# Kernel tuning notes

Measured on AMD Instinct MI355X. Metric: run time of the kernel, lower is better.

The kernel has to match this reference:

```python
import jax, jax.numpy as jnp
import numpy as np

DIM = 2048
H = 16
HD = 128
S = 2640          # frame_seq_len(22*40=880) * num_frame_per_block(3)
CACHE = 5280      # 6 cached frames
MAXPOS = 8192
EPS = 1e-6


def rmsnorm(x, g, eps=EPS):
    return x * jax.lax.rsqrt(jnp.mean(x * x, axis=-1, keepdims=True) + eps) * g


def apply_rope_interleaved(x, cos, sin):
    # x: [s, H, HD]; cos/sin: [s, HD//2]; is_neox=False -> adjacent pairs
    x1 = x[..., 0::2]
    x2 = x[..., 1::2]
    c = cos[:, None, :]
    s_ = sin[:, None, :]
    o1 = x1 * c - x2 * s_
    o2 = x2 * c + x1 * s_
    return jnp.stack([o1, o2], axis=-1).reshape(x.shape)


def setup_inputs() -> dict:
    key = jax.random.key(0)
    ks = jax.random.split(key, 10)
    w_scale = DIM ** -0.5
    x = jax.random.normal(ks[0], (1, S, DIM), dtype=jnp.float32)
    # cos_sin_cache: [max_pos, HD] = [cos(HD//2) | sin(HD//2)], real rope values
    inv_freq = 1.0 / (10000.0 ** (np.arange(0, HD, 2, dtype=np.float32) / HD))
    t = np.arange(MAXPOS, dtype=np.float32)
    ang = np.outer(t, inv_freq)  # [MAXPOS, HD//2]
    freqs = jnp.asarray(np.concatenate([np.cos(ang), np.sin(ang)], axis=1), dtype=jnp.float32)
    k_cache = jax.random.normal(ks[1], (CACHE, H, HD), dtype=jnp.float32)
    v_cache = jax.random.normal(ks[2], (CACHE, H, HD), dtype=jnp.float32)
    Wq = jax.random.normal(ks[3], (DIM, DIM), dtype=jnp.float32) * w_scale
    Wk = jax.random.normal(ks[4], (DIM, DIM), dtype=jnp.float32) * w_scale
    Wv = jax.random.normal(ks[5], (DIM, DIM), dtype=jnp.float32) * w_scale
    Wo = jax.random.normal(ks[6], (DIM, DIM), dtype=jnp.float32) * w_scale
    bq = jnp.zeros((DIM,), jnp.float32)
    bk = jnp.zeros((DIM,), jnp.float32)
    bv = jnp.zeros((DIM,), jnp.float32)
    bo = jnp.zeros((DIM,), jnp.float32)
    gq = jnp.ones((DIM,), jnp.float32)
    gk = jnp.ones((DIM,), jnp.float32)
    return {"x": x, "freqs": freqs, "k_cache": k_cache, "v_cache": v_cache,
            "Wq": Wq, "bq": bq, "Wk": Wk, "bk": bk, "Wv": Wv, "bv": bv,
            "Wo": Wo, "bo": bo, "gq": gq, "gk": gk, "current_start": CACHE}


def reference(x, freqs, k_cache, v_cache, Wq, bq, Wk, bk, Wv, bv, Wo, bo, gq, gk, current_start):
    s = x.shape[1]
    xf = x[0]                                   # [s, DIM], B==1
    q = rmsnorm(xf @ Wq.T + bq, gq).reshape(s, H, HD)
    k = rmsnorm(xf @ Wk.T + bk, gk).reshape(s, H, HD)
    v = (xf @ Wv.T + bv).reshape(s, H, HD)
    # fused RoPE via cos_sin_cache lookup, interleaved (is_neox=False)
    positions = jnp.arange(s, dtype=jnp.int32) + current_start
    cs = freqs[positions]                       # [s, HD]
    cos, sin = cs[:, : HD // 2], cs[:, HD // 2:]
    rq = apply_rope_interleaved(q, cos, sin)
    rk = apply_rope_interleaved(k, cos, sin)
    # streaming attention: full access to cache, causal within incoming block
    k_all = jnp.concatenate([k_cache, rk], axis=0)  # [L, H, HD]
    v_all = jnp.concatenate([v_cache, v], axis=0)
    L = k_all.shape[0]
    scale = HD ** -0.5
    scores = jnp.einsum("qhd,khd->hqk", rq, k_all) * scale  # [H, s, L]
    kv_idx = jnp.arange(L)
    q_idx = jnp.arange(s)
    mask = (kv_idx[None, :] - (L - s)) <= q_idx[:, None]    # cache always visible
    scores = jnp.where(mask[None, :, :], scores, jnp.float32(-1e30))
    attn = jax.nn.softmax(scores, axis=-1)
    out = jnp.einsum("hqk,khd->qhd", attn, v_all).reshape(s, DIM)
    y = out @ Wo.T + bo
    return y[None]                              # [1, s, DIM]
```

## Files before the change

### kernel.cpp

```cpp
#include <hip/hip_runtime.h>

#define DIMN 2048
#define NH 16
#define HDIM 128

typedef __attribute__((ext_vector_type(4))) float f32x4;
typedef __attribute__((ext_vector_type(8))) __bf16 bfx8;
typedef __attribute__((ext_vector_type(8))) unsigned short u16x8;
typedef __attribute__((ext_vector_type(2))) unsigned int u32x2;

__device__ __forceinline__ unsigned short f2bf(float f){
  unsigned u = __builtin_bit_cast(unsigned, f);
  u += 0x7fffu + ((u >> 16) & 1u);
  return (unsigned short)(u >> 16);
}
__device__ __forceinline__ float bf2f(unsigned short h){
  unsigned u = (unsigned)h << 16;
  return __builtin_bit_cast(float, u);
}
__device__ __forceinline__ unsigned cvt_pk_bf16(float lo, float hi){
  unsigned r;
  asm("v_cvt_pk_bf16_f32 %0, %1, %2" : "=v"(r) : "v"(lo), "v"(hi));
  return r;
}

__device__ __forceinline__ void gl_lds16(const void* g, void* l){
  __builtin_amdgcn_global_load_lds((const __attribute__((address_space(1))) void*)g,
                                   (__attribute__((address_space(3))) void*)l, 16, 0, 0);
}

#define MFMA16(a,b,c) __builtin_amdgcn_mfma_f32_16x16x32_bf16((a),(b),(c),0,0,0)

__global__ __launch_bounds__(256) void cast_bf16_kernel(const float* __restrict__ in,
                                                        unsigned short* __restrict__ out, int n8){
  int i = blockIdx.x*256 + threadIdx.x;
  if (i >= n8) return;
  const float4* p = (const float4*)(in + (size_t)i*8);
  float4 a = p[0], b = p[1];
  u16x8 o;
  o[0]=f2bf(a.x); o[1]=f2bf(a.y); o[2]=f2bf(a.z); o[3]=f2bf(a.w);
  o[4]=f2bf(b.x); o[5]=f2bf(b.y); o[6]=f2bf(b.z); o[7]=f2bf(b.w);
  *(u16x8*)(out + (size_t)i*8) = o;
}

__global__ __launch_bounds__(256) void kcache_kernel(const float* __restrict__ kc,
                                                     unsigned short* __restrict__ kb,
                                                     int R, int L_){
  const int gid = blockIdx.x*256 + threadIdx.x;
  if (gid >= R*256) return;
  const size_t idx = (size_t)gid * 8;
  const int k   = (int)(idx >> 11);
  const int rem = (int)(idx & 2047);
  const int hh  = rem >> 7, d = rem & 127;
  const float4* p = (const float4*)(kc + idx);
  float4 a = p[0], b = p[1];
  u16x8 o;
  o[0]=f2bf(a.x); o[1]=f2bf(a.y); o[2]=f2bf(a.z); o[3]=f2bf(a.w);
  o[4]=f2bf(b.x); o[5]=f2bf(b.y); o[6]=f2bf(b.z); o[7]=f2bf(b.w);
  *(u16x8*)(kb + (size_t)hh*L_*HDIM + (size_t)k*HDIM + d) = o;
}

__global__ __launch_bounds__(256) void vtrans_kernel(const float* __restrict__ src,
                                                     unsigned short* __restrict__ vt,
                                                     int R, int koff, int L_){
  __shared__ __align__(16) unsigned short tile[32][72];
  const int kb0 = blockIdx.x * 64, db0 = blockIdx.y * 32, hh = blockIdx.z;
  const int t = threadIdx.x;
  const int kk = t >> 2, dd = (t & 3) * 8;
  const int k = kb0 + kk;
  if (k < R){
    const float* p = src + (size_t)k*DIMN + hh*HDIM + db0 + dd;
    float4 a = ((const float4*)p)[0], b = ((const float4*)p)[1];
    tile[dd+0][kk] = f2bf(a.x); tile[dd+1][kk] = f2bf(a.y);
    tile[dd+2][kk] = f2bf(a.z); tile[dd+3][kk] = f2bf(a.w);
    tile[dd+4][kk] = f2bf(b.x); tile[dd+5][kk] = f2bf(b.y);
    tile[dd+6][kk] = f2bf(b.z); tile[dd+7][kk] = f2bf(b.w);
  }
  __syncthreads();
  const int d = t >> 3, k0 = (t & 7) * 8;
  unsigned short* dst = vt + (size_t)hh*HDIM*L_ + (size_t)(db0+d)*L_ + koff + kb0 + k0;
  if (kb0 + k0 + 8 <= R){
    *(u16x8*)dst = *(const u16x8*)&tile[d][k0];
  } else {
    #pragma unroll
    for (int e=0;e<8;++e) if (kb0 + k0 + e < R) dst[e] = tile[d][k0+e];
  }
}

__global__ __launch_bounds__(256) void vtrans_bf16_kernel(const unsigned short* __restrict__ src,
    unsigned short* __restrict__ vt, int R, int koff, int L_){
  __shared__ __align__(16) unsigned short tile[32][72];
  const int kb0 = blockIdx.x * 64, db0 = blockIdx.y * 32, hh = blockIdx.z;
  const int t = threadIdx.x;
  const int kk = t >> 2, dd = (t & 3) * 8;
  const int k = kb0 + kk;
  if (k < R){
    u16x8 a = *(const u16x8*)(src + (size_t)k*DIMN + hh*HDIM + db0 + dd);
    #pragma unroll
    for (int e=0;e<8;++e) tile[dd+e][kk] = a[e];
  }
  __syncthreads();
  const int d = t >> 3, k0 = (t & 7) * 8;
  unsigned short* dst = vt + (size_t)hh*HDIM*L_ + (size_t)(db0+d)*L_ + koff + kb0 + k0;
  if (kb0 + k0 + 8 <= R){
    *(u16x8*)dst = *(const u16x8*)&tile[d][k0];
  } else {
    #pragma unroll
    for (int e=0;e<8;++e) if (kb0 + k0 + e < R) dst[e] = tile[d][k0+e];
  }
}

__global__ __launch_bounds__(256) void norm_rope_kernel(const unsigned short* __restrict__ lin,
    const float* __restrict__ g, const float* __restrict__ freqs, const int* __restrict__ cur,
    unsigned short* __restrict__ out, int S_, size_t head_stride, int row_off, float oscale){
  const int q = blockIdx.x, t = threadIdx.x;
  u16x8 v = *(const u16x8*)(lin + (size_t)q*DIMN + t*8);
  float x[8];
  #pragma unroll
  for (int e=0;e<8;++e) x[e] = bf2f(v[e]);
  float ss = 0.f;
  #pragma unroll
  for (int e=0;e<8;++e) ss += x[e]*x[e];
  for (int m=1;m<64;m<<=1) ss += __shfl_xor(ss, m);
  __shared__ float red[4];
  if ((t & 63) == 0) red[t>>6] = ss;
  __syncthreads();
  const float tot = red[0]+red[1]+red[2]+red[3];
  const float rstd = rsqrtf(tot * (1.0f/2048.0f) + 1e-6f);
  const int n0 = t*8;
  float xr[8];
  #pragma unroll
  for (int e=0;e<8;++e) xr[e] = x[e] * rstd * g[n0+e];
  const int pos = cur[0] + q;
  const int hh = n0 >> 7, d0 = n0 & 127;
  const float* fr = freqs + (size_t)pos * HDIM;
  float o[8];
  #pragma unroll
  for (int p=0;p<4;++p){
    const int j = (d0>>1) + p;
    const float c = fr[j], s = fr[64+j];
    o[2*p]   = xr[2*p]*c - xr[2*p+1]*s;
    o[2*p+1] = xr[2*p+1]*c + xr[2*p]*s;
  }
  u16x8 ov;
  #pragma unroll
  for (int e=0;e<8;++e) ov[e] = f2bf(o[e]*oscale);
  *(u16x8*)(out + (size_t)hh*head_stride + (size_t)(q+row_off)*HDIM + d0) = ov;
}

__global__ __launch_bounds__(256,2) void gemm_bt(const unsigned short* __restrict__ A,
    const unsigned short* __restrict__ B, const float* __restrict__ bias,
    float* __restrict__ C, int M, int N, int K){
  __shared__ __align__(16) unsigned short As[128*64];
  __shared__ __align__(16) unsigned short Bs[128*64];
  const int t = threadIdx.x;
  const int w = t >> 6, lane = t & 63, lh = lane >> 4, ll = lane & 15;
  const int wr = w >> 1, wc = w & 1;
  const int m0 = blockIdx.y * 128, n0 = blockIdx.x * 128;
  const int srow = t >> 3;
  const int scb  = (t & 7) * 16;
  const int swc  = (scb ^ ((srow & 7) << 4)) >> 1;
  int arow[4]; size_t brow[4];
  #pragma unroll
  for (int c=0;c<4;++c){
    int r = m0 + c*32 + srow; if (r >= M) r = M-1;
    arow[c] = r;
    brow[c] = (size_t)(n0 + c*32 + srow);
  }
  const int xsw = (ll & 7) << 4;
  f32x4 acc[4][4] = {};
  const int nk = K >> 6;
  for (int kt = 0; kt < nk; ++kt){
    const int k0 = kt << 6;
    #pragma unroll
    for (int c=0;c<4;++c){
      gl_lds16(A + (size_t)arow[c]*K + k0 + swc, (char*)As + c*4096 + w*1024);
      gl_lds16(B + brow[c]*K       + k0 + swc, (char*)Bs + c*4096 + w*1024);
    }
    asm volatile("s_waitcnt vmcnt(0)" ::: "memory");
    __syncthreads();
    #pragma unroll
    for (int kk=0;kk<2;++kk){
      const int cb = kk*64 + lh*16;
      bfx8 a[4], b[4];
      #pragma unroll
      for (int i=0;i<4;++i)
        a[i] = *(const bfx8*)((const char*)As + (wr*64 + i*16 + ll)*128 + (cb ^ xsw));
      #pragma unroll
      for (int j=0;j<4;++j)
        b[j] = *(const bfx8*)((const char*)Bs + (wc*64 + j*16 + ll)*128 + (cb ^ xsw));
      #pragma unroll
      for (int i=0;i<4;++i)
        #pragma unroll
        for (int j=0;j<4;++j)
          acc[i][j] = MFMA16(a[i], b[j], acc[i][j]);
    }
    __syncthreads();
  }
  #pragma unroll
  for (int i=0;i<4;++i){
    #pragma unroll
    for (int j=0;j<4;++j){
      const int col = n0 + wc*64 + j*16 + ll;
      const float bb = bias[col];
      #pragma unroll
      for (int r=0;r<4;++r){
        const int row = m0 + wr*64 + i*16 + lh*4 + r;
        if (row < M) C[(size_t)row*N + col] = acc[i][j][r] + bb;
      }
    }
  }
}

__global__ __launch_bounds__(256,2) void gemm_qkv(const unsigned short* __restrict__ A,
    const unsigned short* __restrict__ B0, const unsigned short* __restrict__ B1,
    const unsigned short* __restrict__ B2, const float* __restrict__ g0,
    const float* __restrict__ g1, const float* __restrict__ g2,
    unsigned short* __restrict__ C0, unsigned short* __restrict__ C1,
    unsigned short* __restrict__ C2, int M, int N, int K){
  const int zz = blockIdx.z;
  const unsigned short* B = (zz==0) ? B0 : (zz==1) ? B1 : B2;
  const float* bias       = (zz==0) ? g0 : (zz==1) ? g1 : g2;
  unsigned short* C       = (zz==0) ? C0 : (zz==1) ? C1 : C2;
  __shared__ __align__(16) unsigned short As[128*64];
  __shared__ __align__(16) unsigned short Bs[128*64];
  const int t = threadIdx.x;
  const int w = t >> 6, lane = t & 63, lh = lane >> 4, ll = lane & 15;
  const int wr = w >> 1, wc = w & 1;
  const int m0 = blockIdx.y * 128, n0 = blockIdx.x * 128;
  const int srow = t >> 3;
  const int scb  = (t & 7) * 16;
  const int swc  = (scb ^ ((srow & 7) << 4)) >> 1;
  int arow[4]; size_t brow[4];
  #pragma unroll
  for (int c=0;c<4;++c){
    int r = m0 + c*32 + srow; if (r >= M) r = M-1;
    arow[c] = r;
    brow[c] = (size_t)(n0 + c*32 + srow);
  }
  const int xsw = (ll & 7) << 4;
  f32x4 acc[4][4] = {};
  const int nk = K >> 6;
  for (int kt = 0; kt < nk; ++kt){
    const int k0 = kt << 6;
    #pragma unroll
    for (int c=0;c<4;++c){
      gl_lds16(A + (size_t)arow[c]*K + k0 + swc, (char*)As + c*4096 + w*1024);
      gl_lds16(B + brow[c]*K       + k0 + swc, (char*)Bs + c*4096 + w*1024);
    }
    asm volatile("s_waitcnt vmcnt(0)" ::: "memory");
    __syncthreads();
    #pragma unroll
    for (int kk=0;kk<2;++kk){
      const int cb = kk*64 + lh*16;
      bfx8 a[4], b[4];
      #pragma unroll
      for (int i=0;i<4;++i)
        a[i] = *(const bfx8*)((const char*)As + (wr*64 + i*16 + ll)*128 + (cb ^ xsw));
      #pragma unroll
      for (int j=0;j<4;++j)
        b[j] = *(const bfx8*)((const char*)Bs + (wc*64 + j*16 + ll)*128 + (cb ^ xsw));
      #pragma unroll
      for (int i=0;i<4;++i)
        #pragma unroll
        for (int j=0;j<4;++j)
          acc[i][j] = MFMA16(a[i], b[j], acc[i][j]);
    }
    __syncthreads();
  }
  #pragma unroll
  for (int i=0;i<4;++i){
    #pragma unroll
    for (int j=0;j<4;++j){
      const int col = n0 + wc*64 + j*16 + ll;
      const float bb = bias[col];
      #pragma unroll
      for (int r=0;r<4;++r){
        const int row = m0 + wr*64 + i*16 + lh*4 + r;
        if (row < M) C[(size_t)row*N + col] = f2bf(acc[i][j][r] + bb);
      }
    }
  }
}

__global__ __launch_bounds__(256,2) void attn_kernel(const unsigned short* __restrict__ Q,
    const unsigned short* __restrict__ K, const unsigned short* __restrict__ VT,
    unsigned short* __restrict__ O, float* __restrict__ pacc, float* __restrict__ pml,
    int S_, int L_, int CLn, int nx, int nsplit){
  __shared__ __align__(16) unsigned short Ks[2][64*128];
  __shared__ __align__(16) unsigned short Vs[2][128*64];
  __shared__ __align__(16) unsigned short Ps[4][32*64];
  const int nwg = gridDim.x;
  const int swzid = (blockIdx.x & 7)*(nwg >> 3) + (blockIdx.x >> 3);
  const int xq = swzid % nx;
  const int rest = swzid / nx;
  const int hh = rest % NH;
  const int z  = rest / NH;
  const int q0 = xq * 128;
  const int t = threadIdx.x, w = t >> 6, lane = t & 63, lh = lane >> 4, ll = lane & 15;
  const int xsw = (ll & 7) << 4;
  char* Pw = (char*)Ps[w];
  const unsigned short* Qh = Q  + (size_t)hh*S_*HDIM;
  const unsigned short* Kh = K  + (size_t)hh*L_*HDIM;
  const unsigned short* Vh = VT + (size_t)hh*HDIM*L_;
  bfx8 qf[2][4];
  #pragma unroll
  for (int i=0;i<2;++i){
    int qr = q0 + w*32 + i*16 + ll; if (qr >= S_) qr = S_ - 1;
    #pragma unroll
    for (int kk=0;kk<4;++kk)
      qf[i][kk] = *(const bfx8*)(Qh + (size_t)qr*HDIM + kk*32 + lh*8);
  }
  f32x4 acc[2][8] = {};
  float m_st[2], l_st[2];
  m_st[0] = m_st[1] = -1e20f;
  l_st[0] = l_st[1] = 0.f;
  const int wrow0 = q0 + w*32;
  int qlast = q0 + 127; if (qlast >= S_) qlast = S_ - 1;
  const int kend = CLn + qlast + 1;
  const int nt = (kend + 63) >> 6;
  const int tps = (nt + nsplit - 1) / nsplit;
  const int t0 = z * tps;
  int t1 = t0 + tps; if (t1 > nt) t1 = nt;
  const int ksrow = t >> 4, kchunk = t & 15;
  const int vsrow = t >> 3, vchunk = t & 7;
  const int myq[2] = { wrow0 + ll, wrow0 + 16 + ll };

  u16x8 kreg[4], vreg[4];
  auto load_tile = [&](int ktile){
    const int kv0 = ktile << 6;
    #pragma unroll
    for (int c=0;c<4;++c){
      int krow = kv0 + c*16 + ksrow; if (krow >= L_) krow = L_ - 1;
      kreg[c] = *(const u16x8*)(Kh + (size_t)krow*HDIM + kchunk*8);
      int vcol = kv0 + vchunk*8; if (vcol > L_ - 8) vcol = L_ - 8;
      vreg[c] = *(const u16x8*)(Vh + (size_t)(c*32 + vsrow)*L_ + vcol);
    }
  };
  auto stage_write = [&](int b){
    #pragma unroll
    for (int c=0;c<4;++c){
      *(u16x8*)((char*)Ks[b] + (c*16 + ksrow)*256 + ((kchunk*16) ^ ((ksrow & 7) << 4))) = kreg[c];
      *(u16x8*)((char*)Vs[b] + (c*32 + vsrow)*128 + ((vchunk*16) ^ ((vsrow & 7) << 4))) = vreg[c];
    }
  };
  if (t0 < t1){
    load_tile(t0);
    stage_write(0);
    if (t0 + 1 < t1) load_tile(t0 + 1);
  }
  int cur = 0;
  for (int kt = t0; kt < t1; ++kt){
    const int kv0 = kt << 6;
    __syncthreads();
    const char* Kc = (const char*)Ks[cur];
    const char* Vc = (const char*)Vs[cur];
    f32x4 sc[2][4] = {};
    #pragma unroll
    for (int kk=0;kk<4;++kk){
      const int cb = kk*64 + lh*16;
      #pragma unroll
      for (int j=0;j<4;++j){
        bfx8 kf = *(const bfx8*)(Kc + (j*16 + ll)*256 + (cb ^ xsw));
        sc[0][j] = MFMA16(kf, qf[0][kk], sc[0][j]);
        sc[1][j] = MFMA16(kf, qf[1][kk], sc[1][j]);
      }
    }
    if (kt + 1 < t1){
      stage_write(cur ^ 1);
      if (kt + 2 < t1) load_tile(kt + 2);
    }
    const bool needmask = (kv0 + 63 > CLn + wrow0);
    if (needmask){
      #pragma unroll
      for (int i=0;i<2;++i){
        const int lim = CLn + myq[i];
        #pragma unroll
        for (int j=0;j<4;++j)
          #pragma unroll
          for (int r=0;r<4;++r){
            const int key = kv0 + j*16 + lh*4 + r;
            if (key > lim) sc[i][j][r] = -1e30f;
          }
      }
    }
    float m_t[2];
    #pragma unroll
    for (int i=0;i<2;++i){
      float mt = sc[i][0][0];
      #pragma unroll
      for (int j=0;j<4;++j)
        #pragma unroll
        for (int r=0;r<4;++r) mt = fmaxf(mt, sc[i][j][r]);
      mt = fmaxf(mt, __shfl_xor(mt, 16));
      mt = fmaxf(mt, __shfl_xor(mt, 32));
      m_t[i] = fmaxf(mt, -1e20f);
    }
    const float mdiff = fmaxf(m_t[0] - m_st[0], m_t[1] - m_st[1]);
    if (!__all(mdiff <= 11.54f)){
      float corr[2];
      #pragma unroll
      for (int i=0;i<2;++i){
        const float mn = fmaxf(m_st[i], m_t[i]);
        corr[i] = exp2f(m_st[i] - mn);
        m_st[i] = mn;
        l_st[i] *= corr[i];
      }
      #pragma unroll
      for (int i=0;i<2;++i)
        #pragma unroll
        for (int r=0;r<4;++r){
          const float ca = __shfl(corr[i], lh*4 + r);
          #pragma unroll
          for (int jn=0;jn<8;++jn) acc[i][jn][r] *= ca;
        }
    }
    #pragma unroll
    for (int i=0;i<2;++i){
      float rs = 0.f;
      #pragma unroll
      for (int j=0;j<4;++j)
        #pragma unroll
        for (int r=0;r<4;++r){
          const float pv = exp2f(sc[i][j][r] - m_st[i]);
          sc[i][j][r] = pv;
          rs += pv;
        }
      rs += __shfl_xor(rs, 16);
      rs += __shfl_xor(rs, 32);
      l_st[i] += rs;
    }
    #pragma unroll
    for (int i=0;i<2;++i)
      #pragma unroll
      for (int j=0;j<4;++j){
        u32x2 pk;
        pk[0] = cvt_pk_bf16(sc[i][j][0], sc[i][j][1]);
        pk[1] = cvt_pk_bf16(sc[i][j][2], sc[i][j][3]);
        *(u32x2*)(Pw + (i*16 + ll)*128 + ((j*32 + lh*8) ^ xsw)) = pk;
      }
    #pragma unroll
    for (int kk=0;kk<2;++kk){
      const int cb = kk*64 + lh*16;
      bfx8 af0 = *(const bfx8*)(Pw + (ll)*128      + (cb ^ xsw));
      bfx8 af1 = *(const bfx8*)(Pw + (16 + ll)*128 + (cb ^ xsw));
      #pragma unroll
      for (int jn=0;jn<8;++jn){
        bfx8 vf = *(const bfx8*)(Vc + (jn*16 + ll)*128 + (cb ^ xsw));
        acc[0][jn] = MFMA16(af0, vf, acc[0][jn]);
        acc[1][jn] = MFMA16(af1, vf, acc[1][jn]);
      }
    }
    cur ^= 1;
  }
  if (nsplit == 1){
    #pragma unroll
    for (int i=0;i<2;++i){
      const float linv = 1.0f / l_st[i];
      #pragma unroll
      for (int r=0;r<4;++r){
        const float inv = __shfl(linv, lh*4 + r);
        const int qr = wrow0 + i*16 + lh*4 + r;
        if (qr < S_){
          #pragma unroll
          for (int jn=0;jn<8;++jn)
            O[(size_t)qr*DIMN + hh*HDIM + jn*16 + ll] = f2bf(acc[i][jn][r]*inv);
        }
      }
    }
  } else {
    #pragma unroll
    for (int i=0;i<2;++i){
      #pragma unroll
      for (int r=0;r<4;++r){
        const int qr = wrow0 + i*16 + lh*4 + r;
        if (qr < S_){
          const size_t rid = ((size_t)z*NH + hh)*S_ + qr;
          float* dst = pacc + rid*128;
          #pragma unroll
          for (int jn=0;jn<8;++jn) dst[jn*16 + ll] = acc[i][jn][r];
        }
      }
      if (lane < 16){
        const int qr2 = myq[i];
        if (qr2 < S_){
          const size_t rid2 = ((size_t)z*NH + hh)*S_ + qr2;
          pml[rid2*2]   = m_st[i];
          pml[rid2*2+1] = l_st[i];
        }
      }
    }
  }
}

__global__ __launch_bounds__(256) void combine_kernel(const float* __restrict__ pacc,
    const float* __restrict__ pml, unsigned short* __restrict__ ob, int S_, int nsplit){
  const int t = threadIdx.x;
  const int rid = blockIdx.x*2 + (t >> 7);
  if (rid >= S_*NH) return;
  const int d = t & 127;
  const int hh = rid / S_;
  const int q  = rid - hh*S_;
  float M = -1e20f;
  for (int s=0; s<nsplit; ++s)
    M = fmaxf(M, pml[((size_t)s*NH*S_ + rid)*2]);
  float lt = 0.f, o = 0.f;
  for (int s=0; s<nsplit; ++s){
    const float m = pml[((size_t)s*NH*S_ + rid)*2];
    const float l = pml[((size_t)s*NH*S_ + rid)*2 + 1];
    const float wgt = exp2f(m - M);
    lt += l * wgt;
    o  += pacc[((size_t)s*NH*S_ + rid)*128 + d] * wgt;
  }
  if (lt == 0.f) lt = 1.f;
  ob[(size_t)q*DIMN + hh*HDIM + d] = f2bf(o / lt);
}

extern "C" void kernel_launch(void* const* d_in, const int* in_sizes, int n_in,
                              void* d_out, int out_size, void* d_ws, size_t ws_size,
                              hipStream_t stream){
  const float* x       = (const float*)d_in[0];
  const float* freqs   = (const float*)d_in[1];
  const float* k_cache = (const float*)d_in[2];
  const float* v_cache = (const float*)d_in[3];
  const float* Wq = (const float*)d_in[4];
  const float* bq = (const float*)d_in[5];
  const float* Wk = (const float*)d_in[6];
  const float* bk = (const float*)d_in[7];
  const float* Wv = (const float*)d_in[8];
  const float* bv = (const float*)d_in[9];
  const float* Wo = (const float*)d_in[10];
  const float* bo = (const float*)d_in[11];
  const float* gq = (const float*)d_in[12];
  const float* gk = (const float*)d_in[13];
  const int*   cur = (const int*)d_in[14];

  const int S = in_sizes[0] / DIMN;
  const int CACHE_ = in_sizes[2] / DIMN;
  const int L = CACHE_ + S;
  const int CLn = L - S;

  auto al = [](size_t n){ return (n + 255) & ~(size_t)255; };
  char* base = (char*)d_ws;
  size_t off = 0;
  auto take = [&](size_t n){ char* r = base + off; off += al(n); return r; };
  unsigned short* xb  = (unsigned short*)take((size_t)S*DIMN*2);
  unsigned short* Wob = (unsigned short*)take((size_t)DIMN*DIMN*2);
  unsigned short* qb  = (unsigned short*)take((size_t)NH*S*HDIM*2);
  unsigned short* kb  = (unsigned short*)take((size_t)NH*L*HDIM*2);
  unsigned short* vtb = (unsigned short*)take((size_t)NH*HDIM*L*2);
  unsigned short* ob  = (unsigned short*)take((size_t)S*DIMN*2);
  const size_t ubase = off;
  const size_t l_sz = al((size_t)S*DIMN*2);
  const size_t w_sz = al((size_t)DIMN*DIMN*2);
  unsigned short* lin0 = (unsigned short*)(base + ubase);
  unsigned short* lin1 = (unsigned short*)(base + ubase + l_sz);
  unsigned short* lin2 = (unsigned short*)(base + ubase + 2*l_sz);
  unsigned short* Wqb  = (unsigned short*)(base + ubase + 3*l_sz);
  unsigned short* Wkb  = (unsigned short*)(base + ubase + 3*l_sz + w_sz);
  unsigned short* Wvb  = (unsigned short*)(base + ubase + 3*l_sz + 2*w_sz);
  const size_t trans_sz = 3*l_sz + 3*w_sz;
  auto pool_sz = [&](int ns){
    return al((size_t)ns*NH*S*HDIM*4) + al((size_t)ns*NH*S*2*4);
  };
  int nsplit = 1;
  if (ubase + (trans_sz > pool_sz(4) ? trans_sz : pool_sz(4)) <= ws_size) nsplit = 4;
  else if (ubase + (trans_sz > pool_sz(2) ? trans_sz : pool_sz(2)) <= ws_size) nsplit = 2;
  if (ubase + trans_sz > ws_size) return;
  float* pacc = (float*)(base + ubase);
  float* pml  = (float*)(base + ubase + al((size_t)nsplit*NH*S*HDIM*4));

  const int wn8 = DIMN*DIMN/8;
  cast_bf16_kernel<<<(S*DIMN/8+255)/256, 256, 0, stream>>>(x,  xb,  S*DIMN/8);
  cast_bf16_kernel<<<(wn8+255)/256, 256, 0, stream>>>(Wq, Wqb, wn8);
  cast_bf16_kernel<<<(wn8+255)/256, 256, 0, stream>>>(Wk, Wkb, wn8);
  cast_bf16_kernel<<<(wn8+255)/256, 256, 0, stream>>>(Wv, Wvb, wn8);
  cast_bf16_kernel<<<(wn8+255)/256, 256, 0, stream>>>(Wo, Wob, wn8);
  kcache_kernel<<<CACHE_, 256, 0, stream>>>(k_cache, kb, CACHE_, L);
  vtrans_kernel<<<dim3((CACHE_+63)/64, 4, NH), 256, 0, stream>>>(v_cache, vtb, CACHE_, 0, L);

  const int mb = (S+127)/128;
  gemm_qkv<<<dim3(DIMN/128, mb, 3), 256, 0, stream>>>(xb, Wqb, Wkb, Wvb, bq, bk, bv,
                                                      lin0, lin1, lin2, S, DIMN, DIMN);
  const float qsc = 0.08838834764831845f * 1.4426950408889634f;
  norm_rope_kernel<<<S, 256, 0, stream>>>(lin0, gq, freqs, cur, qb, S, (size_t)S*HDIM, 0, qsc);
  norm_rope_kernel<<<S, 256, 0, stream>>>(lin1, gk, freqs, cur, kb, S, (size_t)L*HDIM, CACHE_, 1.0f);
  vtrans_bf16_kernel<<<dim3((S+63)/64, 4, NH), 256, 0, stream>>>(lin2, vtb, S, CACHE_, L);

  const int nx = (S+127)/128;
  attn_kernel<<<nx*NH*nsplit, 256, 0, stream>>>(qb, kb, vtb, ob,
                                                pacc, pml, S, L, CLn, nx, nsplit);
  if (nsplit > 1)
    combine_kernel<<<(S*NH+1)/2, 256, 0, stream>>>(pacc, pml, ob, S, nsplit);
  gemm_bt<<<dim3(DIMN/128, mb), 256, 0, stream>>>(ob, Wob, bo, (float*)d_out, S, DIMN, DIMN);
}
```

Measured before the change: 514.0 us.

## Single-buffer attention K/V LDS with staggered loads to fit three blocks per CU

Replaces the double-buffered K and V shared-memory tiles in the attention kernel with single buffers. K and V loads are staggered through one register set: V for the next tile is written after QK^T, and K after PV, with an extra barrier between them. This cuts LDS and register use so that three workgroups can be resident per CU instead of two. Bounds clamping is also dropped for non-last tiles. The cost is an additional __syncthreads per iteration and less distance between each global load and its use.

New measurement: 659.3 us. +28.3%, slower.

```diff
diff --git a/kernel.cpp b/kernel.cpp
--- a/kernel.cpp
+++ b/kernel.cpp
@@ -283,12 +283,12 @@
   }
 }
 
-__global__ __launch_bounds__(256,2) void attn_kernel(const unsigned short* __restrict__ Q,
+__global__ __launch_bounds__(256,3) void attn_kernel(const unsigned short* __restrict__ Q,
     const unsigned short* __restrict__ K, const unsigned short* __restrict__ VT,
     unsigned short* __restrict__ O, float* __restrict__ pacc, float* __restrict__ pml,
     int S_, int L_, int CLn, int nx, int nsplit){
-  __shared__ __align__(16) unsigned short Ks[2][64*128];
-  __shared__ __align__(16) unsigned short Vs[2][128*64];
+  __shared__ __align__(16) unsigned short Ks[64*128];
+  __shared__ __align__(16) unsigned short Vs[128*64];
   __shared__ __align__(16) unsigned short Ps[4][32*64];
   const int nwg = gridDim.x;
   const int swzid = (blockIdx.x & 7)*(nwg >> 3) + (blockIdx.x >> 3);
@@ -325,51 +325,62 @@
   const int ksrow = t >> 4, kchunk = t & 15;
   const int vsrow = t >> 3, vchunk = t & 7;
   const int myq[2] = { wrow0 + ll, wrow0 + 16 + ll };
-
-  u16x8 kreg[4], vreg[4];
-  auto load_tile = [&](int ktile){
+  const int last = nt - 1;
+
+  u16x8 sreg[4];
+  auto load_K = [&](int ktile){
     const int kv0 = ktile << 6;
-    #pragma unroll
-    for (int c=0;c<4;++c){
-      int krow = kv0 + c*16 + ksrow; if (krow >= L_) krow = L_ - 1;
-      kreg[c] = *(const u16x8*)(Kh + (size_t)krow*HDIM + kchunk*8);
-      int vcol = kv0 + vchunk*8; if (vcol > L_ - 8) vcol = L_ - 8;
-      vreg[c] = *(const u16x8*)(Vh + (size_t)(c*32 + vsrow)*L_ + vcol);
+    if (ktile == last){
+      #pragma unroll
+      for (int c=0;c<4;++c){
+        int krow = kv0 + c*16 + ksrow; if (krow >= L_) krow = L_ - 1;
+        sreg[c] = *(const u16x8*)(Kh + (size_t)krow*HDIM + kchunk*8);
+      }
+    } else {
+      #pragma unroll
+      for (int c=0;c<4;++c)
+        sreg[c] = *(const u16x8*)(Kh + (size_t)(kv0 + c*16 + ksrow)*HDIM + kchunk*8);
     }
   };
-  auto stage_write = [&](int b){
-    #pragma unroll
-    for (int c=0;c<4;++c){
-      *(u16x8*)((char*)Ks[b] + (c*16 + ksrow)*256 + ((kchunk*16) ^ ((ksrow & 7) << 4))) = kreg[c];
-      *(u16x8*)((char*)Vs[b] + (c*32 + vsrow)*128 + ((vchunk*16) ^ ((vsrow & 7) << 4))) = vreg[c];
-    }
+  auto load_V = [&](int ktile){
+    const int kv0 = ktile << 6;
+    int vcol = kv0 + vchunk*8;
+    if (ktile == last && vcol > L_ - 8) vcol = L_ - 8;
+    #pragma unroll
+    for (int c=0;c<4;++c)
+      sreg[c] = *(const u16x8*)(Vh + (size_t)(c*32 + vsrow)*L_ + vcol);
   };
+  auto write_K = [&](){
+    #pragma unroll
+    for (int c=0;c<4;++c)
+      *(u16x8*)((char*)Ks + (c*16 + ksrow)*256 + ((kchunk*16) ^ ((ksrow & 7) << 4))) = sreg[c];
+  };
+  auto write_V = [&](){
+    #pragma unroll
+    for (int c=0;c<4;++c)
+      *(u16x8*)((char*)Vs + (c*32 + vsrow)*128 + ((vchunk*16) ^ ((vsrow & 7) << 4))) = sreg[c];
+  };
+
   if (t0 < t1){
-    load_tile(t0);
-    stage_write(0);
-    if (t0 + 1 < t1) load_tile(t0 + 1);
-  }
-  int cur = 0;
+    load_K(t0); write_K();
+    load_V(t0);
+  }
   for (int kt = t0; kt < t1; ++kt){
     const int kv0 = kt << 6;
     __syncthreads();
-    const char* Kc = (const char*)Ks[cur];
-    const char* Vc = (const char*)Vs[cur];
     f32x4 sc[2][4] = {};
     #pragma unroll
     for (int kk=0;kk<4;++kk){
       const int cb = kk*64 + lh*16;
       #pragma unroll
       for (int j=0;j<4;++j){
-        bfx8 kf = *(const bfx8*)(Kc + (j*16 + ll)*256 + (cb ^ xsw));
+        bfx8 kf = *(const bfx8*)((const char*)Ks + (j*16 + ll)*256 + (cb ^ xsw));
         sc[0][j] = MFMA16(kf, qf[0][kk], sc[0][j]);
         sc[1][j] = MFMA16(kf, qf[1][kk], sc[1][j]);
       }
     }
-    if (kt + 1 < t1){
-      stage_write(cur ^ 1);
-      if (kt + 2 < t1) load_tile(kt + 2);
-    }
+    write_V();
+    if (kt + 1 < t1) load_K(kt + 1);
     const bool needmask = (kv0 + 63 > CLn + wrow0);
     if (needmask){
       #pragma unroll
@@ -430,6 +441,7 @@
       rs += __shfl_xor(rs, 32);
       l_st[i] += rs;
     }
+    __syncthreads();
     #pragma unroll
     for (int i=0;i<2;++i)
       #pragma unroll
@@ -446,12 +458,15 @@
       bfx8 af1 = *(const bfx8*)(Pw + (16 + ll)*128 + (cb ^ xsw));
       #pragma unroll
       for (int jn=0;jn<8;++jn){
-        bfx8 vf = *(const bfx8*)(Vc + (jn*16 + ll)*128 + (cb ^ xsw));
+        bfx8 vf = *(const bfx8*)((const char*)Vs + (jn*16 + ll)*128 + (cb ^ xsw));
         acc[0][jn] = MFMA16(af0, vf, acc[0][jn]);
         acc[1][jn] = MFMA16(af1, vf, acc[1][jn]);
       }
     }
-    cur ^= 1;
+    if (kt + 1 < t1){
+      write_K();
+      load_V(kt + 1);
+    }
   }
   if (nsplit == 1){
     #pragma unroll
```

## Use 8 waves of 16 query rows each in attention kernel

Applied to the files above, without the earlier changes.

Restructures the attention workgroup from 4 waves × 32 query rows to 8 waves × 16 query rows (512 threads). Each wave keeps half the accumulators, score registers and softmax state, and the K/V staging per thread is halved. The non-last tiles skip the bounds clamps on their loads. The intent is to lower register pressure and raise the number of resident waves to hide latency, at the cost of each K/V LDS fragment being reused across fewer query rows per wave, which means more LDS reads per MFMA.

Result: no change. 524.0 us (+1.9%).

```diff
diff --git a/kernel.cpp b/kernel.cpp
--- a/kernel.cpp
+++ b/kernel.cpp
@@ -6,8 +6,8 @@
 
 typedef __attribute__((ext_vector_type(4))) float f32x4;
 typedef __attribute__((ext_vector_type(8))) __bf16 bfx8;
+typedef __attribute__((ext_vector_type(4))) __bf16 bf16x4;
 typedef __attribute__((ext_vector_type(8))) unsigned short u16x8;
-typedef __attribute__((ext_vector_type(2))) unsigned int u32x2;
 
 __device__ __forceinline__ unsigned short f2bf(float f){
   unsigned u = __builtin_bit_cast(unsigned, f);
@@ -17,11 +17,6 @@
 __device__ __forceinline__ float bf2f(unsigned short h){
   unsigned u = (unsigned)h << 16;
   return __builtin_bit_cast(float, u);
-}
-__device__ __forceinline__ unsigned cvt_pk_bf16(float lo, float hi){
-  unsigned r;
-  asm("v_cvt_pk_bf16_f32 %0, %1, %2" : "=v"(r) : "v"(lo), "v"(hi));
-  return r;
 }
 
 __device__ __forceinline__ void gl_lds16(const void* g, void* l){
@@ -283,13 +278,13 @@
   }
 }
 
-__global__ __launch_bounds__(256,2) void attn_kernel(const unsigned short* __restrict__ Q,
+__global__ __launch_bounds__(512,4) void attn_kernel(const unsigned short* __restrict__ Q,
     const unsigned short* __restrict__ K, const unsigned short* __restrict__ VT,
     unsigned short* __restrict__ O, float* __restrict__ pacc, float* __restrict__ pml,
     int S_, int L_, int CLn, int nx, int nsplit){
   __shared__ __align__(16) unsigned short Ks[2][64*128];
   __shared__ __align__(16) unsigned short Vs[2][128*64];
-  __shared__ __align__(16) unsigned short Ps[4][32*64];
+  __shared__ __align__(16) unsigned short Ps[8][16*64];
   const int nwg = gridDim.x;
   const int swzid = (blockIdx.x & 7)*(nwg >> 3) + (blockIdx.x >> 3);
   const int xq = swzid % nx;
@@ -303,19 +298,16 @@
   const unsigned short* Qh = Q  + (size_t)hh*S_*HDIM;
   const unsigned short* Kh = K  + (size_t)hh*L_*HDIM;
   const unsigned short* Vh = VT + (size_t)hh*HDIM*L_;
-  bfx8 qf[2][4];
-  #pragma unroll
-  for (int i=0;i<2;++i){
-    int qr = q0 + w*32 + i*16 + ll; if (qr >= S_) qr = S_ - 1;
+  const int wrow0 = q0 + w*16;
+  bfx8 qf[4];
+  {
+    int qr = wrow0 + ll; if (qr >= S_) qr = S_ - 1;
     #pragma unroll
     for (int kk=0;kk<4;++kk)
-      qf[i][kk] = *(const bfx8*)(Qh + (size_t)qr*HDIM + kk*32 + lh*8);
-  }
-  f32x4 acc[2][8] = {};
-  float m_st[2], l_st[2];
-  m_st[0] = m_st[1] = -1e20f;
-  l_st[0] = l_st[1] = 0.f;
-  const int wrow0 = q0 + w*32;
+      qf[kk] = *(const bfx8*)(Qh + (size_t)qr*HDIM + kk*32 + lh*8);
+  }
+  f32x4 acc[8] = {};
+  float m_st = -1e20f, l_st = 0.f;
   int qlast = q0 + 127; if (qlast >= S_) qlast = S_ - 1;
   const int kend = CLn + qlast + 1;
   const int nt = (kend + 63) >> 6;
@@ -324,26 +316,41 @@
   int t1 = t0 + tps; if (t1 > nt) t1 = nt;
   const int ksrow = t >> 4, kchunk = t & 15;
   const int vsrow = t >> 3, vchunk = t & 7;
-  const int myq[2] = { wrow0 + ll, wrow0 + 16 + ll };
-
-  u16x8 kreg[4], vreg[4];
+  const int myq = wrow0 + ll;
+  const int last = nt - 1;
+
+  u16x8 kreg[2], vreg[2];
   auto load_tile = [&](int ktile){
     const int kv0 = ktile << 6;
-    #pragma unroll
-    for (int c=0;c<4;++c){
-      int krow = kv0 + c*16 + ksrow; if (krow >= L_) krow = L_ - 1;
-      kreg[c] = *(const u16x8*)(Kh + (size_t)krow*HDIM + kchunk*8);
+    if (ktile == last){
+      #pragma unroll
+      for (int c=0;c<2;++c){
+        int krow = kv0 + c*32 + ksrow; if (krow >= L_) krow = L_ - 1;
+        kreg[c] = *(const u16x8*)(Kh + (size_t)krow*HDIM + kchunk*8);
+      }
       int vcol = kv0 + vchunk*8; if (vcol > L_ - 8) vcol = L_ - 8;
-      vreg[c] = *(const u16x8*)(Vh + (size_t)(c*32 + vsrow)*L_ + vcol);
+      #pragma unroll
+      for (int c=0;c<2;++c)
+        vreg[c] = *(const u16x8*)(Vh + (size_t)(c*64 + vsrow)*L_ + vcol);
+    } else {
+      #pragma unroll
+      for (int c=0;c<2;++c)
+        kreg[c] = *(const u16x8*)(Kh + (size_t)(kv0 + c*32 + ksrow)*HDIM + kchunk*8);
+      const int vcol = kv0 + vchunk*8;
+      #pragma unroll
+      for (int c=0;c<2;++c)
+        vreg[c] = *(const u16x8*)(Vh + (size_t)(c*64 + vsrow)*L_ + vcol);
     }
   };
   auto stage_write = [&](int b){
     #pragma unroll
-    for (int c=0;c<4;++c){
-      *(u16x8*)((char*)Ks[b] + (c*16 + ksrow)*256 + ((kchunk*16) ^ ((ksrow & 7) << 4))) = kreg[c];
-      *(u16x8*)((char*)Vs[b] + (c*32 + vsrow)*128 + ((vchunk*16) ^ ((vsrow & 7) << 4))) = vreg[c];
-    }
+    for (int c=0;c<2;++c)
+      *(u16x8*)((char*)Ks[b] + (c*32 + ksrow)*256 + ((kchunk*16) ^ ((ksrow & 7) << 4))) = kreg[c];
+    #pragma unroll
+    for (int c=0;c<2;++c)
+      *(u16x8*)((char*)Vs[b] + (c*64 + vsrow)*128 + ((vchunk*16) ^ ((vsrow & 7) << 4))) = vreg[c];
   };
+
   if (t0 < t1){
     load_tile(t0);
     stage_write(0);
@@ -355,139 +362,107 @@
     __syncthreads();
     const char* Kc = (const char*)Ks[cur];
     const char* Vc = (const char*)Vs[cur];
-    f32x4 sc[2][4] = {};
+    f32x4 sc[4] = {};
     #pragma unroll
     for (int kk=0;kk<4;++kk){
       const int cb = kk*64 + lh*16;
       #pragma unroll
       for (int j=0;j<4;++j){
         bfx8 kf = *(const bfx8*)(Kc + (j*16 + ll)*256 + (cb ^ xsw));
-        sc[0][j] = MFMA16(kf, qf[0][kk], sc[0][j]);
-        sc[1][j] = MFMA16(kf, qf[1][kk], sc[1][j]);
+        sc[j] = MFMA16(kf, qf[kk], sc[j]);
       }
     }
     if (kt + 1 < t1){
       stage_write(cur ^ 1);
       if (kt + 2 < t1) load_tile(kt + 2);
     }
-    const bool needmask = (kv0 + 63 > CLn + wrow0);
-    if (needmask){
-      #pragma unroll
-      for (int i=0;i<2;++i){
-        const int lim = CLn + myq[i];
-        #pragma unroll
-        for (int j=0;j<4;++j)
-          #pragma unroll
-          for (int r=0;r<4;++r){
-            const int key = kv0 + j*16 + lh*4 + r;
-            if (key > lim) sc[i][j][r] = -1e30f;
-          }
-      }
-    }
-    float m_t[2];
-    #pragma unroll
-    for (int i=0;i<2;++i){
-      float mt = sc[i][0][0];
-      #pragma unroll
-      for (int j=0;j<4;++j)
-        #pragma unroll
-        for (int r=0;r<4;++r) mt = fmaxf(mt, sc[i][j][r]);
-      mt = fmaxf(mt, __shfl_xor(mt, 16));
-      mt = fmaxf(mt, __shfl_xor(mt, 32));
-      m_t[i] = fmaxf(mt, -1e20f);
-    }
-    const float mdiff = fmaxf(m_t[0] - m_st[0], m_t[1] - m_st[1]);
-    if (!__all(mdiff <= 11.54f)){
-      float corr[2];
-      #pragma unroll
-      for (int i=0;i<2;++i){
-        const float mn = fmaxf(m_st[i], m_t[i]);
-        corr[i] = exp2f(m_st[i] - mn);
-        m_st[i] = mn;
-        l_st[i] *= corr[i];
-      }
-      #pragma unroll
-      for (int i=0;i<2;++i)
-        #pragma unroll
-        for (int r=0;r<4;++r){
-          const float ca = __shfl(corr[i], lh*4 + r);
-          #pragma unroll
-          for (int jn=0;jn<8;++jn) acc[i][jn][r] *= ca;
-        }
-    }
-    #pragma unroll
-    for (int i=0;i<2;++i){
-      float rs = 0.f;
+    if (kv0 + 63 > CLn + wrow0){
+      const int lim = CLn + myq;
       #pragma unroll
       for (int j=0;j<4;++j)
         #pragma unroll
         for (int r=0;r<4;++r){
-          const float pv = exp2f(sc[i][j][r] - m_st[i]);
-          sc[i][j][r] = pv;
-          rs += pv;
+          const int key = kv0 + j*16 + lh*4 + r;
+          if (key > lim) sc[j][r] = -1e30f;
         }
-      rs += __shfl_xor(rs, 16);
-      rs += __shfl_xor(rs, 32);
-      l_st[i] += rs;
-    }
-    #pragma unroll
-    for (int i=0;i<2;++i)
-      #pragma unroll
-      for (int j=0;j<4;++j){
-        u32x2 pk;
-        pk[0] = cvt_pk_bf16(sc[i][j][0], sc[i][j][1]);
-        pk[1] = cvt_pk_bf16(sc[i][j][2], sc[i][j][3]);
-        *(u32x2*)(Pw + (i*16 + ll)*128 + ((j*32 + lh*8) ^ xsw)) = pk;
-      }
+    }
+    float mt = sc[0][0];
+    #pragma unroll
+    for (int j=0;j<4;++j)
+      #pragma unroll
+      for (int r=0;r<4;++r) mt = fmaxf(mt, sc[j][r]);
+    mt = fmaxf(mt, __shfl_xor(mt, 16));
+    mt = fmaxf(mt, __shfl_xor(mt, 32));
+    mt = fmaxf(mt, -1e20f);
+    if (!__all(mt - m_st <= 11.54f)){
+      const float mn = fmaxf(m_st, mt);
+      const float corr = exp2f(m_st - mn);
+      m_st = mn;
+      l_st *= corr;
+      #pragma unroll
+      for (int r=0;r<4;++r){
+        const float ca = __shfl(corr, lh*4 + r);
+        #pragma unroll
+        for (int jn=0;jn<8;++jn) acc[jn][r] *= ca;
+      }
+    }
+    float rs = 0.f;
+    #pragma unroll
+    for (int j=0;j<4;++j)
+      #pragma unroll
+      for (int r=0;r<4;++r){
+        const float pv = exp2f(sc[j][r] - m_st);
+        sc[j][r] = pv;
+        rs += pv;
+      }
+    rs += __shfl_xor(rs, 16);
+    rs += __shfl_xor(rs, 32);
+    l_st += rs;
+    #pragma unroll
+    for (int j=0;j<4;++j){
+      bf16x4 pk = { (__bf16)sc[j][0], (__bf16)sc[j][1], (__bf16)sc[j][2], (__bf16)sc[j][3] };
+      *(bf16x4*)(Pw + ll*128 + ((j*32 + lh*8) ^ xsw)) = pk;
+    }
     #pragma unroll
     for (int kk=0;kk<2;++kk){
       const int cb = kk*64 + lh*16;
-      bfx8 af0 = *(const bfx8*)(Pw + (ll)*128      + (cb ^ xsw));
-      bfx8 af1 = *(const bfx8*)(Pw + (16 + ll)*128 + (cb ^ xsw));
+      bfx8 af = *(const bfx8*)(Pw + ll*128 + (cb ^ xsw));
       #pragma unroll
       for (int jn=0;jn<8;++jn){
         bfx8 vf = *(const bfx8*)(Vc + (jn*16 + ll)*128 + (cb ^ xsw));
-        acc[0][jn] = MFMA16(af0, vf, acc[0][jn]);
-        acc[1][jn] = MFMA16(af1, vf, acc[1][jn]);
+        acc[jn] = MFMA16(af, vf, acc[jn]);
       }
     }
     cur ^= 1;
   }
   if (nsplit == 1){
-    #pragma unroll
-    for (int i=0;i<2;++i){
-      const float linv = 1.0f / l_st[i];
-      #pragma unroll
-      for (int r=0;r<4;++r){
-        const float inv = __shfl(linv, lh*4 + r);
-        const int qr = wrow0 + i*16 + lh*4 + r;
-        if (qr < S_){
-          #pragma unroll
-          for (int jn=0;jn<8;++jn)
-            O[(size_t)qr*DIMN + hh*HDIM + jn*16 + ll] = f2bf(acc[i][jn][r]*inv);
-        }
+    const float linv = 1.0f / l_st;
+    #pragma unroll
+    for (int r=0;r<4;++r){
+      const float inv = __shfl(linv, lh*4 + r);
+      const int qr = wrow0 + lh*4 + r;
+      if (qr < S_){
+        #pragma unroll
+        for (int jn=0;jn<8;++jn)
+          O[(size_t)qr*DIMN + hh*HDIM + jn*16 + ll] = f2bf(acc[jn][r]*inv);
       }
     }
   } else {
     #pragma unroll
-    for (int i=0;i<2;++i){
-      #pragma unroll
-      for (int r=0;r<4;++r){
-        const int qr = wrow0 + i*16 + lh*4 + r;
-        if (qr < S_){
-          const size_t rid = ((size_t)z*NH + hh)*S_ + qr;
-          float* dst = pacc + rid*128;
-          #pragma unroll
-          for (int jn=0;jn<8;++jn) dst[jn*16 + ll] = acc[i][jn][r];
-        }
-      }
-      if (lane < 16){
-        const int qr2 = myq[i];
-        if (qr2 < S_){
-          const size_t rid2 = ((size_t)z*NH + hh)*S_ + qr2;
-          pml[rid2*2]   = m_st[i];
-          pml[rid2*2+1] = l_st[i];
-        }
+    for (int r=0;r<4;++r){
+      const int qr = wrow0 + lh*4 + r;
+      if (qr < S_){
+        const size_t rid = ((size_t)z*NH + hh)*S_ + qr;
+        float* dst = pacc + rid*128;
+        #pragma unroll
+        for (int jn=0;jn<8;++jn) dst[jn*16 + ll] = acc[jn][r];
+      }
+    }
+    if (lane < 16){
+      if (myq < S_){
+        const size_t rid2 = ((size_t)z*NH + hh)*S_ + myq;
+        pml[rid2*2]   = m_st;
+        pml[rid2*2+1] = l_st;
       }
     }
   }
@@ -588,7 +563,7 @@
   vtrans_bf16_kernel<<<dim3((S+63)/64, 4, NH), 256, 0, stream>>>(lin2, vtb, S, CACHE_, L);
 
   const int nx = (S+127)/128;
-  attn_kernel<<<nx*NH*nsplit, 256, 0, stream>>>(qb, kb, vtb, ob,
+  attn_kernel<<<nx*NH*nsplit, 512, 0, stream>>>(qb, kb, vtb, ob,
                                                 pacc, pml, S, L, CLn, nx, nsplit);
   if (nsplit > 1)
     combine_kernel<<<(S*NH+1)/2, 256, 0, stream>>>(pacc, pml, ob, S, nsplit);
```
